# Kernel tuning notes

Hardware: AMD Instinct MI355X
Metric: run time of the kernel (lower is better)

The kernel has to match this reference:

```python
import jax, jax.numpy as jnp
import numpy as np

F_DIM = 256
NEG = -(2.0**15) + 1.0  # mask fill value, applied BEFORE scaling as in the original
EPS = 1e-5


def _lin(x, W, b):
    # nn.Linear: y = x @ W.T + b, W: [out, in]
    return jnp.einsum('...i,oi->...o', x, W) + b


def _ln(x):
    # LayerNorm over last dim, no affine
    m = jnp.mean(x, axis=-1, keepdims=True)
    v = jnp.var(x, axis=-1, keepdims=True)
    return (x - m) * jax.lax.rsqrt(v + EPS)


def setup_inputs() -> dict:
    key = jax.random.key(0)
    ks = jax.random.split(key, 16)
    B, T, N, F = 8, 96, 400, F_DIM
    s = 1.0 / np.sqrt(F)
    inp = {
        'xl': jax.random.normal(ks[0], (B, T, N, F), jnp.float32),
        'xh': jax.random.normal(ks[1], (B, T, N, F), jnp.float32),
        'te': jax.random.normal(ks[2], (B, T, 1, F), jnp.float32),
        'Wq': jax.random.normal(ks[3], (F, F), jnp.float32) * s,
        'bq': jnp.zeros((F,), jnp.float32),
        'Wk': jax.random.normal(ks[4], (F, F), jnp.float32) * s,
        'bk': jnp.zeros((F,), jnp.float32),
        'Wv': jax.random.normal(ks[5], (F, F), jnp.float32) * s,
        'bv': jnp.zeros((F,), jnp.float32),
        'Wo': jax.random.normal(ks[6], (F, F), jnp.float32) * s,
        'bo': jnp.zeros((F,), jnp.float32),
        'Wf1': jax.random.normal(ks[7], (F, F), jnp.float32) * s,
        'bf1': jnp.zeros((F,), jnp.float32),
        'Wf2': jax.random.normal(ks[8], (F, F), jnp.float32) * s,
        'bf2': jnp.zeros((F,), jnp.float32),
    }
    return inp


def reference(xl, xh, te, Wq, bq, Wk, bk, Wv, bv, Wo, bo, Wf1, bf1, Wf2, bf2):
    B, T, N, F = xl.shape
    xl = xl + te[:, -T:]           # broadcast te over N
    xh = xh + te[:, -T:]
    q = _lin(xl, Wq, bq).transpose(0, 2, 1, 3)              # [B,N,T,F]
    k = jax.nn.relu(_lin(xh, Wk, bk)).transpose(0, 2, 1, 3)  # [B,N,T,F]
    v = jax.nn.relu(_lin(xh, Wv, bv)).transpose(0, 2, 1, 3)  # [B,N,T,F]
    scores = jnp.einsum('bntf,bnsf->bnts', q, k)            # [B,N,T,T]
    causal = jnp.tril(jnp.ones((T, T), bool))
    scores = jnp.where(causal, scores, NEG)                  # mask BEFORE scaling (matches torch code)
    scores = scores / jnp.sqrt(jnp.float32(F))
    attn = jax.nn.softmax(scores, axis=-1)
    out = jnp.einsum('bnts,bnsf->bntf', attn, v).transpose(0, 2, 1, 3)  # [B,T,N,F]
    out = _lin(out, Wo, bo)
    out = _ln(out + xl)
    # FeedForward([F,F,F], res_ln=True): linear -> relu -> linear, +residual, LN
    h = jax.nn.relu(_lin(out, Wf1, bf1))
    h = _lin(h, Wf2, bf2)
    return _ln(h + out)
```

## Files before the change

### kernel.cpp

```cpp
#include <hip/hip_runtime.h>
#include <stdint.h>

typedef unsigned short u16;
typedef __bf16 bf16x8 __attribute__((ext_vector_type(8)));
typedef float f32x4 __attribute__((ext_vector_type(4)));

#define B_ 8
#define T_ 96
#define N_ 400
#define F_ 256
#define MROWS (B_*T_*N_)

__device__ __forceinline__ float bf2f(u16 u){
  union { uint32_t i; float f; } c; c.i = ((uint32_t)u) << 16; return c.f;
}
__device__ __forceinline__ u16 f2bf(float x){
  union { float f; uint32_t i; } c; c.f = x;
  uint32_t u = c.i;
  u = (u + 0x7FFFu + ((u >> 16) & 1u)) >> 16;
  return (u16)u;
}

__device__ __forceinline__ void gll16(const void* g, void* l){
  __builtin_amdgcn_global_load_lds((const __attribute__((address_space(1))) uint32_t*)g,
                                   (__attribute__((address_space(3))) uint32_t*)l, 16, 0, 0);
}

__device__ __forceinline__ f32x4 mfma16(bf16x8 a, bf16x8 b, f32x4 c){
  return __builtin_amdgcn_mfma_f32_16x16x32_bf16(a, b, c, 0, 0, 0);
}

__global__ __launch_bounds__(256) void cvtw_k(const float* __restrict__ src, u16* __restrict__ dst){
  int i = (blockIdx.x * 256 + threadIdx.x) * 4;
  float4 v = *(const float4*)(src + i);
  union { u16 h[4]; uint2 u; } o;
  o.h[0] = f2bf(v.x); o.h[1] = f2bf(v.y); o.h[2] = f2bf(v.z); o.h[3] = f2bf(v.w);
  *(uint2*)(dst + i) = o.u;
}

__global__ __launch_bounds__(256) void prep_k(const float* __restrict__ xl, const float* __restrict__ xh,
                                              const float* __restrict__ te,
                                              u16* __restrict__ xl2, u16* __restrict__ xh2){
  long i0 = ((long)blockIdx.x * 256 + threadIdx.x) * 8;
  long row = i0 >> 8; int f = (int)(i0 & 255);
  long tb = (row / N_) * 256 + f;
  float4 t0 = *(const float4*)(te + tb);
  float4 t1 = *(const float4*)(te + tb + 4);
  float4 a0 = *(const float4*)(xl + i0), a1 = *(const float4*)(xl + i0 + 4);
  float4 b0 = *(const float4*)(xh + i0), b1 = *(const float4*)(xh + i0 + 4);
  union { u16 h[8]; uint4 v; } oa, ob;
  oa.h[0]=f2bf(a0.x+t0.x); oa.h[1]=f2bf(a0.y+t0.y); oa.h[2]=f2bf(a0.z+t0.z); oa.h[3]=f2bf(a0.w+t0.w);
  oa.h[4]=f2bf(a1.x+t1.x); oa.h[5]=f2bf(a1.y+t1.y); oa.h[6]=f2bf(a1.z+t1.z); oa.h[7]=f2bf(a1.w+t1.w);
  ob.h[0]=f2bf(b0.x+t0.x); ob.h[1]=f2bf(b0.y+t0.y); ob.h[2]=f2bf(b0.z+t0.z); ob.h[3]=f2bf(b0.w+t0.w);
  ob.h[4]=f2bf(b1.x+t1.x); ob.h[5]=f2bf(b1.y+t1.y); ob.h[6]=f2bf(b1.z+t1.z); ob.h[7]=f2bf(b1.w+t1.w);
  *(uint4*)(xl2 + i0) = oa.v;
  *(uint4*)(xh2 + i0) = ob.v;
}

template<bool RELU, bool LN, bool F32OUT>
__global__ __launch_bounds__(512, 1) void gemm_k(const u16* __restrict__ A, const u16* __restrict__ W,
                                                 const float* __restrict__ bias, const u16* __restrict__ Res,
                                                 void* __restrict__ Out){
  __shared__ u16 lds[128*32 + 256*32];
  const int tid = threadIdx.x;
  const int w = tid >> 6, lane = tid & 63, quad = lane >> 4, l16 = lane & 15;
  const int rw = w & 1, cw = w >> 1;
  const long row0 = (long)blockIdx.x * 128;

  f32x4 acc[4][4];
  #pragma unroll
  for (int i=0;i<4;i++)
    #pragma unroll
    for (int j=0;j<4;j++) acc[i][j] = (f32x4)0.0f;

  for (int ks = 0; ks < 8; ++ks){
    __syncthreads();
    #pragma unroll
    for (int j = 0; j < 3; ++j){
      int c = j*512 + tid;
      const u16* src;
      if (c < 512){ int r = c >> 2, kc = c & 3; src = A + ((row0 + r)*256 + ks*32 + kc*8); }
      else        { int cb = c - 512; int o = cb >> 2, kc = cb & 3; src = W + (o*256 + ks*32 + kc*8); }
      u16* dst = lds + (j*512 + w*64)*8;
      gll16(src, dst);
    }
    __syncthreads();
    bf16x8 af[4], bfp[4];
    #pragma unroll
    for (int rt=0;rt<4;rt++) af[rt]  = *(const bf16x8*)(lds + ((rw*64 + rt*16 + l16)*32 + quad*8));
    #pragma unroll
    for (int ct=0;ct<4;ct++) bfp[ct] = *(const bf16x8*)(lds + 4096 + ((cw*64 + ct*16 + l16)*32 + quad*8));
    #pragma unroll
    for (int rt=0;rt<4;rt++)
      #pragma unroll
      for (int ct=0;ct<4;ct++)
        acc[rt][ct] = mfma16(af[rt], bfp[ct], acc[rt][ct]);
  }

  float bb[4];
  #pragma unroll
  for (int ct=0;ct<4;ct++) bb[ct] = bias[cw*64 + ct*16 + l16];

  #pragma unroll
  for (int rt=0;rt<4;rt++){
    #pragma unroll
    for (int reg=0;reg<4;reg++){
      long grow = row0 + rw*64 + rt*16 + quad*4 + reg;
      #pragma unroll
      for (int ct=0;ct<4;ct++){
        float v = acc[rt][ct][reg] + bb[ct];
        if (RELU) v = fmaxf(v, 0.0f);
        if (LN)   v += bf2f(Res[grow*256 + cw*64 + ct*16 + l16]);
        acc[rt][ct][reg] = v;
      }
    }
  }

  if (!LN){
    u16* o16 = (u16*)Out;
    #pragma unroll
    for (int rt=0;rt<4;rt++)
      #pragma unroll
      for (int reg=0;reg<4;reg++){
        long grow = row0 + rw*64 + rt*16 + quad*4 + reg;
        #pragma unroll
        for (int ct=0;ct<4;ct++)
          o16[grow*256 + cw*64 + ct*16 + l16] = f2bf(acc[rt][ct][reg]);
      }
  } else {
    __syncthreads();
    float* red = (float*)lds;
    float* mr  = red + 1024;
    #pragma unroll
    for (int rt=0;rt<4;rt++){
      #pragma unroll
      for (int reg=0;reg<4;reg++){
        float s = 0.f, s2 = 0.f;
        #pragma unroll
        for (int ct=0;ct<4;ct++){ float v = acc[rt][ct][reg]; s += v; s2 += v*v; }
        #pragma unroll
        for (int m=1;m<16;m<<=1){ s += __shfl_xor(s, m); s2 += __shfl_xor(s2, m); }
        int rl = rw*64 + rt*16 + quad*4 + reg;
        if (l16 == 0){ red[(rl*4 + cw)*2] = s; red[(rl*4 + cw)*2 + 1] = s2; }
      }
    }
    __syncthreads();
    if (tid < 128){
      float s = 0.f, s2 = 0.f;
      #pragma unroll
      for (int i=0;i<4;i++){ s += red[(tid*4 + i)*2]; s2 += red[(tid*4 + i)*2 + 1]; }
      float mean = s * (1.0f/256.0f);
      float var  = s2 * (1.0f/256.0f) - mean*mean;
      mr[tid*2] = mean; mr[tid*2 + 1] = rsqrtf(var + 1e-5f);
    }
    __syncthreads();
    #pragma unroll
    for (int rt=0;rt<4;rt++){
      #pragma unroll
      for (int reg=0;reg<4;reg++){
        int rl = rw*64 + rt*16 + quad*4 + reg;
        long grow = row0 + rl;
        float mean = mr[rl*2], rs = mr[rl*2 + 1];
        #pragma unroll
        for (int ct=0;ct<4;ct++){
          float v = (acc[rt][ct][reg] - mean) * rs;
          if (F32OUT) ((float*)Out)[grow*256 + cw*64 + ct*16 + l16] = v;
          else        ((u16*)Out)[grow*256 + cw*64 + ct*16 + l16] = f2bf(v);
        }
      }
    }
  }
}

__global__ __launch_bounds__(256, 1) void attn_k(const u16* __restrict__ Q, const u16* __restrict__ K,
                                                 const u16* __restrict__ V, u16* __restrict__ O){
  __shared__ u16 sm[26112];
  const int tid = threadIdx.x, w = tid >> 6, lane = tid & 63, quad = lane >> 4, l16 = lane & 15;
  const int n = blockIdx.x % N_, b = blockIdx.x / N_;

  #define GROW(t) (((long)((b)*T_ + (t))*N_ + n)*256)

  bf16x8 aq[2][8];
  #pragma unroll
  for (int rt=0;rt<2;rt++){
    int t = w*32 + rt*16 + l16; if (t > 95) t = 95;
    const u16* qp = Q + GROW(t) + quad*8;
    #pragma unroll
    for (int kf=0;kf<8;kf++) aq[rt][kf] = *(const bf16x8*)(qp + kf*32);
  }

  f32x4 accS[2][8];
  #pragma unroll
  for (int i=0;i<2;i++)
    #pragma unroll
    for (int j=0;j<8;j++) accS[i][j] = (f32x4)0.0f;

  for (int half=0; half<2; ++half){
    __syncthreads();
    #pragma unroll
    for (int it=0; it<8; ++it){
      int idx = it*256 + tid; int s = idx >> 4, fc = idx & 15;
      uint4 val = make_uint4(0u,0u,0u,0u);
      if (s < 96) val = *(const uint4*)(K + GROW(s) + half*128 + fc*8);
      *(uint4*)(sm + s*136 + fc*8) = val;
    }
    __syncthreads();
    #pragma unroll
    for (int ks=0; ks<4; ++ks){
      bf16x8 bk[8];
      #pragma unroll
      for (int ct=0;ct<8;ct++) bk[ct] = *(const bf16x8*)(sm + (ct*16 + l16)*136 + ks*32 + quad*8);
      #pragma unroll
      for (int rt=0;rt<2;rt++)
        #pragma unroll
        for (int ct=0;ct<8;ct++)
          accS[rt][ct] = mfma16(aq[rt][half*4 + ks], bk[ct], accS[rt][ct]);
    }
  }

  __syncthreads();
  const float scale = 0.0625f;
  const float NEGs = -32767.0f * 0.0625f;
  #pragma unroll
  for (int rt=0;rt<2;rt++){
    #pragma unroll
    for (int reg=0;reg<4;reg++){
      int t = w*32 + rt*16 + quad*4 + reg;
      float vals[8];
      float m = -3.4e38f;
      #pragma unroll
      for (int ct=0;ct<8;ct++){
        int s = ct*16 + l16;
        float v = (s <= t) ? accS[rt][ct][reg]*scale : NEGs;
        vals[ct] = v; m = fmaxf(m, v);
      }
      #pragma unroll
      for (int msk=1;msk<16;msk<<=1) m = fmaxf(m, __shfl_xor(m, msk));
      float sum = 0.f;
      #pragma unroll
      for (int ct=0;ct<8;ct++){ float p = __expf(vals[ct] - m); vals[ct] = p; sum += p; }
      #pragma unroll
      for (int msk=1;msk<16;msk<<=1) sum += __shfl_xor(sum, msk);
      float inv = 1.0f / sum;
      #pragma unroll
      for (int ct=0;ct<8;ct++) sm[t*136 + ct*16 + l16] = f2bf(vals[ct]*inv);
    }
  }
  __syncthreads();

  bf16x8 ap[2][4];
  #pragma unroll
  for (int rt=0;rt<2;rt++){
    int t = w*32 + rt*16 + l16;
    #pragma unroll
    for (int ks=0;ks<4;ks++) ap[rt][ks] = *(const bf16x8*)(sm + t*136 + ks*32 + quad*8);
  }

  u16* sv = sm + 17408;
  for (int fq=0; fq<4; ++fq){
    __syncthreads();
    #pragma unroll
    for (int it=0; it<24; ++it){
      int idx = it*256 + tid; int s = idx >> 6, f = idx & 63;
      sv[f*136 + s] = V[GROW(s) + fq*64 + f];
    }
    #pragma unroll
    for (int it=0; it<8; ++it){
      int idx = it*256 + tid; int f = idx >> 5, s = 96 + (idx & 31);
      sv[f*136 + s] = 0;
    }
    __syncthreads();
    f32x4 accO[2][4];
    #pragma unroll
    for (int i=0;i<2;i++)
      #pragma unroll
      for (int j=0;j<4;j++) accO[i][j] = (f32x4)0.0f;
    #pragma unroll
    for (int ks=0;ks<4;ks++){
      bf16x8 bv[4];
      #pragma unroll
      for (int ct=0;ct<4;ct++) bv[ct] = *(const bf16x8*)(sv + (ct*16 + l16)*136 + ks*32 + quad*8);
      #pragma unroll
      for (int rt=0;rt<2;rt++)
        #pragma unroll
        for (int ct=0;ct<4;ct++)
          accO[rt][ct] = mfma16(ap[rt][ks], bv[ct], accO[rt][ct]);
    }
    #pragma unroll
    for (int rt=0;rt<2;rt++)
      #pragma unroll
      for (int reg=0;reg<4;reg++){
        int t = w*32 + rt*16 + quad*4 + reg;
        if (t < 96){
          long gb = GROW(t) + fq*64;
          #pragma unroll
          for (int ct=0;ct<4;ct++) O[gb + ct*16 + l16] = f2bf(accO[rt][ct][reg]);
        }
      }
  }
  #undef GROW
}

extern "C" void kernel_launch(void* const* d_in, const int* in_sizes, int n_in,
                              void* d_out, int out_size, void* d_ws, size_t ws_size,
                              hipStream_t stream){
  const float* xl  = (const float*)d_in[0];
  const float* xh  = (const float*)d_in[1];
  const float* te  = (const float*)d_in[2];
  const float* Wq  = (const float*)d_in[3];  const float* bq  = (const float*)d_in[4];
  const float* Wk  = (const float*)d_in[5];  const float* bk  = (const float*)d_in[6];
  const float* Wv  = (const float*)d_in[7];  const float* bv  = (const float*)d_in[8];
  const float* Wo  = (const float*)d_in[9];  const float* bo  = (const float*)d_in[10];
  const float* Wf1 = (const float*)d_in[11]; const float* bf1 = (const float*)d_in[12];
  const float* Wf2 = (const float*)d_in[13]; const float* bf2 = (const float*)d_in[14];

  u16* ws = (u16*)d_ws;
  const long S1 = (long)MROWS * 256;
  u16* xl2 = ws;
  u16* xh2 = ws + S1;
  u16* qb  = ws + 2*S1;
  u16* kb  = ws + 3*S1;
  u16* vb  = ws + 4*S1;
  u16* wb  = ws + 5*S1;
  u16* wbq = wb, *wbk = wb + 65536, *wbv = wb + 2*65536,
     * wbo = wb + 3*65536, *wbf1 = wb + 4*65536, *wbf2 = wb + 5*65536;

  cvtw_k<<<64, 256, 0, stream>>>(Wq,  wbq);
  cvtw_k<<<64, 256, 0, stream>>>(Wk,  wbk);
  cvtw_k<<<64, 256, 0, stream>>>(Wv,  wbv);
  cvtw_k<<<64, 256, 0, stream>>>(Wo,  wbo);
  cvtw_k<<<64, 256, 0, stream>>>(Wf1, wbf1);
  cvtw_k<<<64, 256, 0, stream>>>(Wf2, wbf2);

  prep_k<<<38400, 256, 0, stream>>>(xl, xh, te, xl2, xh2);

  const int GB = MROWS / 128;
  gemm_k<false,false,false><<<GB, 512, 0, stream>>>(xl2, wbq, bq, nullptr, qb);
  gemm_k<true, false,false><<<GB, 512, 0, stream>>>(xh2, wbk, bk, nullptr, kb);
  gemm_k<true, false,false><<<GB, 512, 0, stream>>>(xh2, wbv, bv, nullptr, vb);

  attn_k<<<B_*N_, 256, 0, stream>>>(qb, kb, vb, xh2);

  gemm_k<false,true, false><<<GB, 512, 0, stream>>>(xh2, wbo, bo, xl2, qb);
  gemm_k<true, false,false><<<GB, 512, 0, stream>>>(qb,  wbf1, bf1, nullptr, kb);
  gemm_k<false,true, true ><<<GB, 512, 0, stream>>>(kb,  wbf2, bf2, qb, d_out);
}
```

Measured before the change: 1.728 ms.

## Reorder rows to (b,n,t) layout and store V transposed for attention

The prep kernel now writes activations in a (b,n,t) row order, so each attention block's 96 rows for one (b,n) sit contiguously. The V projection GEMM writes its output transposed per (b,n) group, and the final LN GEMM scatters rows back to the original (b,t,n) order. Attention loads K and V tiles directly into LDS with global_load_lds and an XOR swizzle, drops the padded 128-row tiles to the exact 96, skips work for the padded Q rows, and raises launch bounds for more occupancy. This replaces the strided gathers and scalar transposed V stores in attention, at the cost of strided writes in the V GEMM epilogue and in the output scatter.

New measurement: 2.302 ms. +33.2%, slower.

```diff
diff --git a/kernel.cpp b/kernel.cpp
--- a/kernel.cpp
+++ b/kernel.cpp
@@ -42,12 +42,14 @@
                                               const float* __restrict__ te,
                                               u16* __restrict__ xl2, u16* __restrict__ xh2){
   long i0 = ((long)blockIdx.x * 256 + threadIdx.x) * 8;
-  long row = i0 >> 8; int f = (int)(i0 & 255);
-  long tb = (row / N_) * 256 + f;
-  float4 t0 = *(const float4*)(te + tb);
-  float4 t1 = *(const float4*)(te + tb + 4);
-  float4 a0 = *(const float4*)(xl + i0), a1 = *(const float4*)(xl + i0 + 4);
-  float4 b0 = *(const float4*)(xh + i0), b1 = *(const float4*)(xh + i0 + 4);
+  int row_o = (int)(i0 >> 8); int f = (int)(i0 & 255);
+  int b = row_o / 38400; int r = row_o - b*38400; int n = r / 96; int t = r - n*96;
+  long ioff = ((long)((b*96 + t)*400 + n))*256 + f;
+  long toff = ((long)(b*96 + t))*256 + f;
+  float4 t0 = *(const float4*)(te + toff);
+  float4 t1 = *(const float4*)(te + toff + 4);
+  float4 a0 = *(const float4*)(xl + ioff), a1 = *(const float4*)(xl + ioff + 4);
+  float4 b0 = *(const float4*)(xh + ioff), b1 = *(const float4*)(xh + ioff + 4);
   union { u16 h[8]; uint4 v; } oa, ob;
   oa.h[0]=f2bf(a0.x+t0.x); oa.h[1]=f2bf(a0.y+t0.y); oa.h[2]=f2bf(a0.z+t0.z); oa.h[3]=f2bf(a0.w+t0.w);
   oa.h[4]=f2bf(a1.x+t1.x); oa.h[5]=f2bf(a1.y+t1.y); oa.h[6]=f2bf(a1.z+t1.z); oa.h[7]=f2bf(a1.w+t1.w);
@@ -57,7 +59,7 @@
   *(uint4*)(xh2 + i0) = ob.v;
 }
 
-template<bool RELU, bool LN, bool F32OUT>
+template<bool RELU, bool LN, bool F32OUT, bool TRANSV>
 __global__ __launch_bounds__(512, 1) void gemm_k(const u16* __restrict__ A, const u16* __restrict__ W,
                                                  const float* __restrict__ bias, const u16* __restrict__ Res,
                                                  void* __restrict__ Out){
@@ -117,16 +119,34 @@
   }
 
   if (!LN){
-    u16* o16 = (u16*)Out;
-    #pragma unroll
-    for (int rt=0;rt<4;rt++)
-      #pragma unroll
-      for (int reg=0;reg<4;reg++){
-        long grow = row0 + rw*64 + rt*16 + quad*4 + reg;
-        #pragma unroll
-        for (int ct=0;ct<4;ct++)
-          o16[grow*256 + cw*64 + ct*16 + l16] = f2bf(acc[rt][ct][reg]);
-      }
+    if (TRANSV){
+      u16* o16 = (u16*)Out;
+      #pragma unroll
+      for (int rt=0;rt<4;rt++){
+        int grow0 = (int)(row0 + rw*64 + rt*16 + quad*4);
+        int bn = grow0 / 96; int t0 = grow0 - bn*96;
+        u16* dstb = o16 + (long)bn*24576 + t0;
+        #pragma unroll
+        for (int ct=0;ct<4;ct++){
+          union { u16 h[4]; uint2 u; } pk;
+          #pragma unroll
+          for (int reg=0;reg<4;reg++) pk.h[reg] = f2bf(acc[rt][ct][reg]);
+          int col = cw*64 + ct*16 + l16;
+          *(uint2*)(dstb + (long)col*96) = pk.u;
+        }
+      }
+    } else {
+      u16* o16 = (u16*)Out;
+      #pragma unroll
+      for (int rt=0;rt<4;rt++)
+        #pragma unroll
+        for (int reg=0;reg<4;reg++){
+          long grow = row0 + rw*64 + rt*16 + quad*4 + reg;
+          #pragma unroll
+          for (int ct=0;ct<4;ct++)
+            o16[grow*256 + cw*64 + ct*16 + l16] = f2bf(acc[rt][ct][reg]);
+        }
+    }
   } else {
     __syncthreads();
     float* red = (float*)lds;
@@ -164,72 +184,85 @@
         #pragma unroll
         for (int ct=0;ct<4;ct++){
           float v = (acc[rt][ct][reg] - mean) * rs;
-          if (F32OUT) ((float*)Out)[grow*256 + cw*64 + ct*16 + l16] = v;
-          else        ((u16*)Out)[grow*256 + cw*64 + ct*16 + l16] = f2bf(v);
+          if (F32OUT){
+            int g = (int)grow; int b = g / 38400; int r = g - b*38400;
+            int n = r / 96; int t = r - n*96;
+            long orow = ((long)((b*96 + t)*400 + n))*256;
+            ((float*)Out)[orow + cw*64 + ct*16 + l16] = v;
+          } else {
+            ((u16*)Out)[grow*256 + cw*64 + ct*16 + l16] = f2bf(v);
+          }
         }
       }
     }
   }
 }
 
-__global__ __launch_bounds__(256, 1) void attn_k(const u16* __restrict__ Q, const u16* __restrict__ K,
+__global__ __launch_bounds__(256, 3) void attn_k(const u16* __restrict__ Q, const u16* __restrict__ K,
                                                  const u16* __restrict__ V, u16* __restrict__ O){
-  __shared__ u16 sm[26112];
+  __shared__ u16 sm[16384 + 96*104];
   const int tid = threadIdx.x, w = tid >> 6, lane = tid & 63, quad = lane >> 4, l16 = lane & 15;
-  const int n = blockIdx.x % N_, b = blockIdx.x / N_;
-
-  #define GROW(t) (((long)((b)*T_ + (t))*N_ + n)*256)
+  const long base = (long)blockIdx.x * 24576;
+  const int NT = (w < 2) ? 2 : 1;
+  u16* smP = sm + 16384;
+
+  #pragma unroll
+  for (int it=0; it<6; ++it){
+    int idx = it*256 + tid; int s = idx >> 4, c = idx & 15;
+    gll16(K + base + s*256 + ((c ^ (s & 7)) * 8), sm + (it*256 + w*64)*8);
+  }
 
   bf16x8 aq[2][8];
-  #pragma unroll
-  for (int rt=0;rt<2;rt++){
-    int t = w*32 + rt*16 + l16; if (t > 95) t = 95;
-    const u16* qp = Q + GROW(t) + quad*8;
-    #pragma unroll
-    for (int kf=0;kf<8;kf++) aq[rt][kf] = *(const bf16x8*)(qp + kf*32);
-  }
-
-  f32x4 accS[2][8];
+  for (int rt=0; rt<2; ++rt){
+    if (rt < NT){
+      int t = (w + rt*4)*16 + l16;
+      const u16* qp = Q + base + t*256 + quad*8;
+      #pragma unroll
+      for (int kf=0;kf<8;kf++) aq[rt][kf] = *(const bf16x8*)(qp + kf*32);
+    }
+  }
+
+  f32x4 accS[2][6];
   #pragma unroll
   for (int i=0;i<2;i++)
     #pragma unroll
-    for (int j=0;j<8;j++) accS[i][j] = (f32x4)0.0f;
-
-  for (int half=0; half<2; ++half){
-    __syncthreads();
-    #pragma unroll
-    for (int it=0; it<8; ++it){
-      int idx = it*256 + tid; int s = idx >> 4, fc = idx & 15;
-      uint4 val = make_uint4(0u,0u,0u,0u);
-      if (s < 96) val = *(const uint4*)(K + GROW(s) + half*128 + fc*8);
-      *(uint4*)(sm + s*136 + fc*8) = val;
+    for (int j=0;j<6;j++) accS[i][j] = (f32x4)0.0f;
+
+  for (int h=0; h<2; ++h){
+    if (h){
+      __syncthreads();
+      #pragma unroll
+      for (int it=0; it<6; ++it){
+        int idx = it*256 + tid; int s = idx >> 4, c = idx & 15;
+        gll16(K + base + s*256 + 128 + ((c ^ (s & 7)) * 8), sm + (it*256 + w*64)*8);
+      }
     }
     __syncthreads();
     #pragma unroll
     for (int ks=0; ks<4; ++ks){
-      bf16x8 bk[8];
-      #pragma unroll
-      for (int ct=0;ct<8;ct++) bk[ct] = *(const bf16x8*)(sm + (ct*16 + l16)*136 + ks*32 + quad*8);
-      #pragma unroll
-      for (int rt=0;rt<2;rt++)
-        #pragma unroll
-        for (int ct=0;ct<8;ct++)
-          accS[rt][ct] = mfma16(aq[rt][half*4 + ks], bk[ct], accS[rt][ct]);
-    }
-  }
-
-  __syncthreads();
+      bf16x8 bk[6];
+      #pragma unroll
+      for (int ct=0;ct<6;ct++){
+        int s = ct*16 + l16;
+        bk[ct] = *(const bf16x8*)(sm + s*128 + (((ks*4 + quad) ^ (s & 7))*8));
+      }
+      for (int rt=0; rt<NT; ++rt)
+        #pragma unroll
+        for (int ct=0;ct<6;ct++)
+          accS[rt][ct] = mfma16(aq[rt][h*4 + ks], bk[ct], accS[rt][ct]);
+    }
+  }
+
   const float scale = 0.0625f;
   const float NEGs = -32767.0f * 0.0625f;
-  #pragma unroll
-  for (int rt=0;rt<2;rt++){
+  for (int rt=0; rt<NT; ++rt){
+    int tl = w + rt*4;
     #pragma unroll
     for (int reg=0;reg<4;reg++){
-      int t = w*32 + rt*16 + quad*4 + reg;
-      float vals[8];
-      float m = -3.4e38f;
-      #pragma unroll
-      for (int ct=0;ct<8;ct++){
+      int t = tl*16 + quad*4 + reg;
+      float vals[6]; float m = -3.4e38f;
+      #pragma unroll
+      for (int ct=0;ct<6;ct++){
         int s = ct*16 + l16;
         float v = (s <= t) ? accS[rt][ct][reg]*scale : NEGs;
         vals[ct] = v; m = fmaxf(m, v);
@@ -238,67 +271,67 @@
       for (int msk=1;msk<16;msk<<=1) m = fmaxf(m, __shfl_xor(m, msk));
       float sum = 0.f;
       #pragma unroll
-      for (int ct=0;ct<8;ct++){ float p = __expf(vals[ct] - m); vals[ct] = p; sum += p; }
+      for (int ct=0;ct<6;ct++){ float p = __expf(vals[ct] - m); vals[ct] = p; sum += p; }
       #pragma unroll
       for (int msk=1;msk<16;msk<<=1) sum += __shfl_xor(sum, msk);
       float inv = 1.0f / sum;
       #pragma unroll
-      for (int ct=0;ct<8;ct++) sm[t*136 + ct*16 + l16] = f2bf(vals[ct]*inv);
+      for (int ct=0;ct<6;ct++) smP[t*104 + ct*16 + l16] = f2bf(vals[ct]*inv);
     }
   }
   __syncthreads();
 
-  bf16x8 ap[2][4];
-  #pragma unroll
-  for (int rt=0;rt<2;rt++){
-    int t = w*32 + rt*16 + l16;
-    #pragma unroll
-    for (int ks=0;ks<4;ks++) ap[rt][ks] = *(const bf16x8*)(sm + t*136 + ks*32 + quad*8);
-  }
-
-  u16* sv = sm + 17408;
-  for (int fq=0; fq<4; ++fq){
-    __syncthreads();
-    #pragma unroll
-    for (int it=0; it<24; ++it){
-      int idx = it*256 + tid; int s = idx >> 6, f = idx & 63;
-      sv[f*136 + s] = V[GROW(s) + fq*64 + f];
-    }
-    #pragma unroll
-    for (int it=0; it<8; ++it){
-      int idx = it*256 + tid; int f = idx >> 5, s = 96 + (idx & 31);
-      sv[f*136 + s] = 0;
-    }
-    __syncthreads();
-    f32x4 accO[2][4];
+  #pragma unroll
+  for (int it=0; it<8; ++it){
+    int idx = it*256 + tid; int fr = idx >> 4, c = idx & 15;
+    gll16(V + base + fr*96 + ((c ^ (fr & 7)) * 8), sm + (it*256 + w*64)*8);
+  }
+  bf16x8 ap[2][3];
+  for (int rt=0; rt<NT; ++rt){
+    int t = (w + rt*4)*16 + l16;
+    #pragma unroll
+    for (int ks=0;ks<3;ks++) ap[rt][ks] = *(const bf16x8*)(smP + t*104 + ks*32 + quad*8);
+  }
+
+  for (int h=0; h<2; ++h){
+    __syncthreads();
+    f32x4 accO[2][8];
     #pragma unroll
     for (int i=0;i<2;i++)
       #pragma unroll
-      for (int j=0;j<4;j++) accO[i][j] = (f32x4)0.0f;
-    #pragma unroll
-    for (int ks=0;ks<4;ks++){
-      bf16x8 bv[4];
-      #pragma unroll
-      for (int ct=0;ct<4;ct++) bv[ct] = *(const bf16x8*)(sv + (ct*16 + l16)*136 + ks*32 + quad*8);
-      #pragma unroll
-      for (int rt=0;rt<2;rt++)
-        #pragma unroll
-        for (int ct=0;ct<4;ct++)
+      for (int j=0;j<8;j++) accO[i][j] = (f32x4)0.0f;
+    #pragma unroll
+    for (int ks=0;ks<3;ks++){
+      bf16x8 bv[8];
+      #pragma unroll
+      for (int ct=0;ct<8;ct++){
+        int fr = ct*16 + l16;
+        bv[ct] = *(const bf16x8*)(sm + fr*128 + (((ks*4 + quad) ^ (fr & 7))*8));
+      }
+      for (int rt=0; rt<NT; ++rt)
+        #pragma unroll
+        for (int ct=0;ct<8;ct++)
           accO[rt][ct] = mfma16(ap[rt][ks], bv[ct], accO[rt][ct]);
     }
-    #pragma unroll
-    for (int rt=0;rt<2;rt++)
+    if (h == 0){
+      __syncthreads();
+      #pragma unroll
+      for (int it=0; it<8; ++it){
+        int idx = it*256 + tid; int fr = idx >> 4, c = idx & 15;
+        gll16(V + base + (128 + fr)*96 + ((c ^ (fr & 7)) * 8), sm + (it*256 + w*64)*8);
+      }
+    }
+    for (int rt=0; rt<NT; ++rt){
+      int tl = w + rt*4;
       #pragma unroll
       for (int reg=0;reg<4;reg++){
-        int t = w*32 + rt*16 + quad*4 + reg;
-        if (t < 96){
-          long gb = GROW(t) + fq*64;
-          #pragma unroll
-          for (int ct=0;ct<4;ct++) O[gb + ct*16 + l16] = f2bf(accO[rt][ct][reg]);
-        }
-      }
-  }
-  #undef GROW
+        int t = tl*16 + quad*4 + reg;
+        long gb = base + t*256 + h*128;
+        #pragma unroll
+        for (int ct=0;ct<8;ct++) O[gb + ct*16 + l16] = f2bf(accO[rt][ct][reg]);
+      }
+    }
+  }
 }
 
 extern "C" void kernel_launch(void* const* d_in, const int* in_sizes, int n_in,
@@ -335,13 +368,13 @@
   prep_k<<<38400, 256, 0, stream>>>(xl, xh, te, xl2, xh2);
 
   const int GB = MROWS / 128;
-  gemm_k<false,false,false><<<GB, 512, 0, stream>>>(xl2, wbq, bq, nullptr, qb);
-  gemm_k<true, false,false><<<GB, 512, 0, stream>>>(xh2, wbk, bk, nullptr, kb);
-  gemm_k<true, false,false><<<GB, 512, 0, stream>>>(xh2, wbv, bv, nullptr, vb);
+  gemm_k<false,false,false,false><<<GB, 512, 0, stream>>>(xl2, wbq, bq, nullptr, qb);
+  gemm_k<true, false,false,false><<<GB, 512, 0, stream>>>(xh2, wbk, bk, nullptr, kb);
+  gemm_k<true, false,false,true ><<<GB, 512, 0, stream>>>(xh2, wbv, bv, nullptr, vb);
 
   attn_k<<<B_*N_, 256, 0, stream>>>(qb, kb, vb, xh2);
 
-  gemm_k<false,true, false><<<GB, 512, 0, stream>>>(xh2, wbo, bo, xl2, qb);
-  gemm_k<true, false,false><<<GB, 512, 0, stream>>>(qb,  wbf1, bf1, nullptr, kb);
-  gemm_k<false,true, true ><<<GB, 512, 0, stream>>>(kb,  wbf2, bf2, qb, d_out);
-}
+  gemm_k<false,true, false,false><<<GB, 512, 0, stream>>>(xh2, wbo, bo, xl2, qb);
+  gemm_k<true, false,false,false><<<GB, 512, 0, stream>>>(qb,  wbf1, bf1, nullptr, kb);
+  gemm_k<false,true, true ,false><<<GB, 512, 0, stream>>>(kb,  wbf2, bf2, qb, d_out);
+}
```
